# Performance work log

Measured on AMD Instinct MI355X. Metric: run time of the kernel, lower is better.

## Reference

```python
import jax, jax.numpy as jnp
import numpy as np

N = 8192          # num nodes
T = 8             # num node types (== num_bases, full basis)
H = 4             # attention heads
IN = 64           # in_feat
OUT = 64          # out_feat


def setup_inputs() -> dict:
    key = jax.random.key(0)
    ks = jax.random.split(key, 9)
    return {
        "agg_msg": jax.random.normal(ks[0], (N, H * IN), dtype=jnp.float32),
        "h": jax.random.normal(ks[1], (N, OUT), dtype=jnp.float32),
        "node_type": jax.random.randint(ks[2], (N,), 0, T),
        "W_att": jax.random.normal(ks[3], (T, H * IN, IN), dtype=jnp.float32) * 0.05,
        "b_att": jax.random.normal(ks[4], (T, OUT), dtype=jnp.float32) * 0.05,
        "W_in": jax.random.normal(ks[5], (T, IN, 3 * OUT), dtype=jnp.float32) * 0.05,
        "W_hid": jax.random.normal(ks[6], (T, OUT, 3 * OUT), dtype=jnp.float32) * 0.05,
        "b_in": jax.random.normal(ks[7], (T, 3 * OUT), dtype=jnp.float32) * 0.05,
        "b_hid": jax.random.normal(ks[8], (T, 3 * OUT), dtype=jnp.float32) * 0.05,
    }


def reference(agg_msg, h, node_type, W_att, b_att, W_in, W_hid, b_in, b_hid):
    # activation on aggregated message (F.relu)
    x = jax.nn.relu(agg_msg)                                 # [N, H*IN]
    # --- attention-head aggregation: per-node-type weight gather + bmm ---
    Wa = W_att[node_type]                                    # [N, H*IN, IN]  (irregular gather)
    x = jnp.einsum('nd,ndo->no', x, Wa) + b_att[node_type]   # [N, IN]
    x = jax.nn.relu(x)
    # --- GRU-style gated update with per-node-type weights ---
    gi = jnp.einsum('ni,nio->no', x, W_in[node_type]) + b_in[node_type]    # [N, 3*OUT]
    gh = jnp.einsum('nk,nko->no', h, W_hid[node_type]) + b_hid[node_type]  # [N, 3*OUT]
    i_r, i_z, i_n = jnp.split(gi, 3, axis=-1)
    h_r, h_z, h_n = jnp.split(gh, 3, axis=-1)
    r = jax.nn.sigmoid(i_r + h_r)
    z = jax.nn.sigmoid(i_z + h_z)
    n = jnp.tanh(i_n + r * h_n)
    h_new = (1.0 - z) * n + z * h                            # [N, OUT]
    return h_new
```

## Files before the change

### kernel.cpp

```cpp
#include <hip/hip_runtime.h>

#define N_NODES 8192
#define T_TYPES 8
#define HIN 256
#define OUTF 64
#define G3 192
#define BM 64
#define MAXBLK 135
#define SCAT_BLKS 32

typedef __attribute__((ext_vector_type(8))) __bf16 bf16x8;
typedef __attribute__((ext_vector_type(4))) float f32x4;

#define WS_CURS 0
#define WS_PERM 256
#define WS_WAT  (256 + 262144)
#define WS_WIT  (WS_WAT + 262144)
#define WS_WHT  (WS_WIT + 196608)
#define WS_CNT  (WS_WHT + 196608)

#define L_XS  0
#define L_WAS 32768
#define L_WIS 65536
#define L_WHS 90112
#define L_YS  114688
#define L_HS  122880
#define L_HF  131072
#define L_IDX 147456
#define L_TOT 147712

#define GLD_LDS16(g, l) __builtin_amdgcn_global_load_lds( \
    (const __attribute__((address_space(1))) void*)(g),   \
    (__attribute__((address_space(3))) void*)(l), 16, 0, 0)

__device__ __forceinline__ unsigned short f2bf(float f) {
    unsigned u = __float_as_uint(f);
    return (unsigned short)((u + 0x7FFFu + ((u >> 16) & 1u)) >> 16);
}
__device__ __forceinline__ int pack2bf(float a, float b) {
    return (int)f2bf(a) | ((int)f2bf(b) << 16);
}

__global__ __launch_bounds__(256) void prep_and_count(
    const float* __restrict__ W_att, const float* __restrict__ W_in,
    const float* __restrict__ W_hid, const int* __restrict__ nt,
    int* __restrict__ counts,
    unsigned short* __restrict__ waT, unsigned short* __restrict__ wiT,
    unsigned short* __restrict__ whT)
{
    __shared__ float Lf[64][68];
    __shared__ int hist[8];
    const int tid = threadIdx.x;
    const int b = blockIdx.x;

    if (b >= 80) {
        int j = b - 80;
        if (tid < 8) hist[tid] = 0;
        __syncthreads();
        atomicAdd(&hist[nt[j * 256 + tid]], 1);
        __syncthreads();
        if (tid < 8) counts[j * 8 + tid] = hist[tid];
        return;
    }

    const float* src;
    unsigned short* dstBase;
    int srcStride, rowBytes, colBase, rBase;

    if (b < 32) {
        int t = b >> 2, kt = b & 3;
        src = W_att + (((size_t)t * 256 + kt * 64) << 6);
        srcStride = 64;
        dstBase = waT + (size_t)t * 16384;
        rowBytes = 512; colBase = kt * 128; rBase = 0;
    } else {
        int j = b - 32;
        int isWh = (j >= 24); if (isWh) j -= 24;
        int t = j / 3, nt2 = j - t * 3;
        src = (isWh ? W_hid : W_in) + (size_t)t * 64 * 192 + nt2 * 64;
        srcStride = 192;
        dstBase = (isWh ? whT : wiT) + (size_t)t * 12288;
        rowBytes = 128; colBase = 0; rBase = nt2 * 64;
    }

    #pragma unroll
    for (int e = 0; e < 4; ++e) {
        int f = e * 256 + tid;
        int kk = f >> 4, c = (f & 15) << 2;
        float4 v = *(const float4*)(src + kk * srcStride + c);
        Lf[kk][c] = v.x; Lf[kk][c + 1] = v.y; Lf[kk][c + 2] = v.z; Lf[kk][c + 3] = v.w;
    }
    __syncthreads();

    #pragma unroll
    for (int e = 0; e < 2; ++e) {
        int q = e * 256 + tid;
        int ko8 = q >> 6, rl = q & 63;
        int r = rBase + rl;
        unsigned short tmp[8];
        #pragma unroll
        for (int j2 = 0; j2 < 8; ++j2)
            tmp[j2] = f2bf(Lf[ko8 * 8 + j2][rl]);
        int4 wv;
        wv.x = (int)tmp[0] | ((int)tmp[1] << 16);
        wv.y = (int)tmp[2] | ((int)tmp[3] << 16);
        wv.z = (int)tmp[4] | ((int)tmp[5] << 16);
        wv.w = (int)tmp[6] | ((int)tmp[7] << 16);
        int B = r * rowBytes + colBase + ((ko8 << 4) ^ ((r & 7) << 4));
        *(int4*)((char*)dstBase + B) = wv;
    }
}

__global__ __launch_bounds__(256) void scatter_pass(
    const int* __restrict__ nt, const int* __restrict__ counts,
    int* __restrict__ cursors, int* __restrict__ perm)
{
    __shared__ int tbl[SCAT_BLKS * 8];
    __shared__ int cur[8];
    const int tid = threadIdx.x;
    const int j = blockIdx.x;

    tbl[tid] = counts[tid];
    __syncthreads();
    if (tid < 8) {
        int base = 0, tot = 0;
        #pragma unroll
        for (int k = 0; k < SCAT_BLKS; ++k) {
            int c = tbl[k * 8 + tid];
            if (k < j) base += c;
            tot += c;
        }
        cur[tid] = base;
        if (j == 0) cursors[tid] = tot;
    }
    __syncthreads();
    int i = j * 256 + tid;
    int t = nt[i];
    int pos = atomicAdd(&cur[t], 1);
    perm[t * N_NODES + pos] = i;
}

__global__ __launch_bounds__(512, 1) void fused_rgnn(
    const float* __restrict__ agg, const float* __restrict__ h,
    const int* __restrict__ cursors, const int* __restrict__ perm,
    const unsigned short* __restrict__ waT, const unsigned short* __restrict__ wiT,
    const unsigned short* __restrict__ whT,
    const float* __restrict__ b_att, const float* __restrict__ b_in,
    const float* __restrict__ b_hid, float* __restrict__ out)
{
    __shared__ __align__(16) char sm_[L_TOT];
    char* sm = sm_;
    const int tid = threadIdx.x;
    const int b = blockIdx.x;

    const int4 c0 = *(const int4*)cursors;
    const int4 c1 = *(const int4*)(cursors + 4);
    const int cntArr[8] = {c0.x, c0.y, c0.z, c0.w, c1.x, c1.y, c1.z, c1.w};
    int t = -1, chunk = 0, tcnt = 0, acc = 0;
    #pragma unroll
    for (int tt = 0; tt < T_TYPES; ++tt) {
        int nc = (cntArr[tt] + BM - 1) >> 6;
        if (t < 0 && b < acc + nc) { t = tt; chunk = b - acc; tcnt = cntArr[tt]; }
        acc += nc;
    }
    if (t < 0) return;
    const int m0 = chunk * BM;
    const int mcnt = min(BM, tcnt - m0);

    const int lane = tid & 63;
    const int w = tid >> 6;
    const int wc = w & 3;
    const int wrh = w >> 2;
    const int lr = lane & 15;
    const int lk = lane >> 4;
    const int col = (wc << 4) + lr;
    const int swzA = (lr & 7) << 4;

    const float ba  = b_att[(t << 6) + col];
    const float bir = b_in [t * G3 + col];
    const float biz = b_in [t * G3 + 64 + col];
    const float bnn = b_in [t * G3 + 128 + col];
    const float bhr = b_hid[t * G3 + col];
    const float bhz = b_hid[t * G3 + 64 + col];
    const float bhn = b_hid[t * G3 + 128 + col];

    const int kx = (tid & 31) << 3;
    const int nbx = tid >> 5;
    int xg[4];
    #pragma unroll
    for (int s = 0; s < 4; ++s) {
        int node = nbx + (s << 4);
        xg[s] = (node < mcnt) ? perm[t * N_NODES + m0 + node] : -1;
    }
    const int nh = tid >> 3;
    const int kh = (tid & 7) << 3;
    int hg = (nh < mcnt) ? perm[t * N_NODES + m0 + nh] : -1;

    float4 xv[4][2];
    #pragma unroll
    for (int s = 0; s < 4; ++s) {
        if (xg[s] >= 0) {
            const float* p = agg + (size_t)xg[s] * HIN + kx;
            xv[s][0] = *(const float4*)p;
            xv[s][1] = *(const float4*)(p + 4);
        } else {
            xv[s][0] = make_float4(0.f, 0.f, 0.f, 0.f);
            xv[s][1] = make_float4(0.f, 0.f, 0.f, 0.f);
        }
    }
    float4 hv0, hv1;
    if (hg >= 0) {
        const float* p = h + (size_t)hg * OUTF + kh;
        hv0 = *(const float4*)p;
        hv1 = *(const float4*)(p + 4);
    } else {
        hv0 = make_float4(0.f, 0.f, 0.f, 0.f);
        hv1 = make_float4(0.f, 0.f, 0.f, 0.f);
    }

    {
        const char* was = (const char*)(waT + (size_t)t * 16384);
        const char* wis = (const char*)(wiT + (size_t)t * 12288);
        const char* whs = (const char*)(whT + (size_t)t * 12288);
        #pragma unroll
        for (int r = 0; r < 4; ++r) {
            int c = (r << 3) + w;
            GLD_LDS16(was + (c << 10) + (lane << 4), sm + L_WAS + (c << 10));
        }
        #pragma unroll
        for (int r = 0; r < 3; ++r) {
            int c = (r << 3) + w;
            GLD_LDS16(wis + (c << 10) + (lane << 4), sm + L_WIS + (c << 10));
            GLD_LDS16(whs + (c << 10) + (lane << 4), sm + L_WHS + (c << 10));
        }
    }

    #pragma unroll
    for (int s = 0; s < 4; ++s) {
        int node = nbx + (s << 4);
        float4 a = xv[s][0], bq = xv[s][1];
        int4 wv;
        wv.x = pack2bf(fmaxf(a.x, 0.f), fmaxf(a.y, 0.f));
        wv.y = pack2bf(fmaxf(a.z, 0.f), fmaxf(a.w, 0.f));
        wv.z = pack2bf(fmaxf(bq.x, 0.f), fmaxf(bq.y, 0.f));
        wv.w = pack2bf(fmaxf(bq.z, 0.f), fmaxf(bq.w, 0.f));
        *(int4*)(sm + L_XS + (node << 9) + ((kx << 1) ^ ((node & 7) << 4))) = wv;
    }
    {
        *(float4*)(sm + L_HF + (nh << 8) + (kh << 2)) = hv0;
        *(float4*)(sm + L_HF + (nh << 8) + (kh << 2) + 16) = hv1;
        int4 wv;
        wv.x = pack2bf(hv0.x, hv0.y);
        wv.y = pack2bf(hv0.z, hv0.w);
        wv.z = pack2bf(hv1.x, hv1.y);
        wv.w = pack2bf(hv1.z, hv1.w);
        *(int4*)(sm + L_HS + (nh << 7) + ((kh << 1) ^ ((nh & 7) << 4))) = wv;
        if ((tid & 7) == 0) ((int*)(sm + L_IDX))[nh] = hg;
    }
    __syncthreads();

    f32x4 yacc[2];
    #pragma unroll
    for (int m = 0; m < 2; ++m) yacc[m] = (f32x4){0.f, 0.f, 0.f, 0.f};
    #pragma unroll
    for (int ks = 0; ks < 8; ++ks) {
        int off = ((ks << 6) + (lk << 4)) ^ swzA;
        bf16x8 bb = *(const bf16x8*)(sm + L_WAS + (((wc << 4) + lr) << 9) + off);
        #pragma unroll
        for (int m = 0; m < 2; ++m) {
            int mt = (wrh << 1) + m;
            bf16x8 am = *(const bf16x8*)(sm + L_XS + (((mt << 4) + lr) << 9) + off);
            yacc[m] = __builtin_amdgcn_mfma_f32_16x16x32_bf16(am, bb, yacc[m], 0, 0, 0);
        }
    }
    #pragma unroll
    for (int m = 0; m < 2; ++m) {
        #pragma unroll
        for (int r = 0; r < 4; ++r) {
            int row = (((wrh << 1) + m) << 4) + (lk << 2) + r;
            float y = fmaxf(yacc[m][r] + ba, 0.f);
            *(unsigned short*)(sm + L_YS + (row << 7) +
                               ((col << 1) ^ ((row & 7) << 4))) = f2bf(y);
        }
    }
    __syncthreads();

    f32x4 gi[2][3], gh[2][3];
    #pragma unroll
    for (int m = 0; m < 2; ++m)
        #pragma unroll
        for (int g = 0; g < 3; ++g) {
            gi[m][g] = (f32x4){0.f, 0.f, 0.f, 0.f};
            gh[m][g] = (f32x4){0.f, 0.f, 0.f, 0.f};
        }
    #pragma unroll
    for (int ks = 0; ks < 2; ++ks) {
        int off = ((ks << 6) + (lk << 4)) ^ swzA;
        bf16x8 ay[2], ah[2];
        #pragma unroll
        for (int m = 0; m < 2; ++m) {
            int mt = (wrh << 1) + m;
            ay[m] = *(const bf16x8*)(sm + L_YS + (((mt << 4) + lr) << 7) + off);
            ah[m] = *(const bf16x8*)(sm + L_HS + (((mt << 4) + lr) << 7) + off);
        }
        #pragma unroll
        for (int g = 0; g < 3; ++g) {
            int brow = (g << 6) + col;
            bf16x8 bi = *(const bf16x8*)(sm + L_WIS + (brow << 7) + off);
            bf16x8 bh = *(const bf16x8*)(sm + L_WHS + (brow << 7) + off);
            #pragma unroll
            for (int m = 0; m < 2; ++m) {
                gi[m][g] = __builtin_amdgcn_mfma_f32_16x16x32_bf16(ay[m], bi, gi[m][g], 0, 0, 0);
                gh[m][g] = __builtin_amdgcn_mfma_f32_16x16x32_bf16(ah[m], bh, gh[m][g], 0, 0, 0);
            }
        }
    }

    const int* idxp = (const int*)(sm + L_IDX);
    #pragma unroll
    for (int m = 0; m < 2; ++m) {
        #pragma unroll
        for (int r = 0; r < 4; ++r) {
            int node = (((wrh << 1) + m) << 4) + (lk << 2) + r;
            if (node < mcnt) {
                int gidx = idxp[node];
                float rv = gi[m][0][r] + bir + gh[m][0][r] + bhr;
                float rg = 1.f / (1.f + __expf(-rv));
                float zv = gi[m][1][r] + biz + gh[m][1][r] + bhz;
                float zg = 1.f / (1.f + __expf(-zv));
                float ng = tanhf(gi[m][2][r] + bnn + rg * (gh[m][2][r] + bhn));
                float hold = *(const float*)(sm + L_HF + (node << 8) + (col << 2));
                out[(size_t)gidx * OUTF + col] = (1.f - zg) * ng + zg * hold;
            }
        }
    }
}

extern "C" void kernel_launch(void* const* d_in, const int* in_sizes, int n_in,
                              void* d_out, int out_size, void* d_ws, size_t ws_size,
                              hipStream_t stream) {
    const float* agg   = (const float*)d_in[0];
    const float* h     = (const float*)d_in[1];
    const int*   ntype = (const int*)d_in[2];
    const float* W_att = (const float*)d_in[3];
    const float* b_att = (const float*)d_in[4];
    const float* W_in  = (const float*)d_in[5];
    const float* W_hid = (const float*)d_in[6];
    const float* b_in  = (const float*)d_in[7];
    const float* b_hid = (const float*)d_in[8];
    float* out = (float*)d_out;

    char* ws = (char*)d_ws;
    int* cursors = (int*)(ws + WS_CURS);
    int* perm = (int*)(ws + WS_PERM);
    unsigned short* waT = (unsigned short*)(ws + WS_WAT);
    unsigned short* wiT = (unsigned short*)(ws + WS_WIT);
    unsigned short* whT = (unsigned short*)(ws + WS_WHT);
    int* counts = (int*)(ws + WS_CNT);

    prep_and_count<<<112, 256, 0, stream>>>(W_att, W_in, W_hid, ntype, counts, waT, wiT, whT);
    scatter_pass<<<SCAT_BLKS, 256, 0, stream>>>(ntype, counts, cursors, perm);
    fused_rgnn<<<MAXBLK, 512, 0, stream>>>(agg, h, cursors, perm,
        waT, wiT, whT, b_att, b_in, b_hid, out);
}
```

Measured before the change: 20.76 us.

## Fold scatter pass into fused kernel by building per-block index list in LDS

```diff
diff --git a/kernel.cpp b/kernel.cpp
--- a/kernel.cpp
+++ b/kernel.cpp
@@ -7,27 +7,28 @@
 #define G3 192
 #define BM 64
 #define MAXBLK 135
-#define SCAT_BLKS 32
 
 typedef __attribute__((ext_vector_type(8))) __bf16 bf16x8;
 typedef __attribute__((ext_vector_type(4))) float f32x4;
 
-#define WS_CURS 0
-#define WS_PERM 256
-#define WS_WAT  (256 + 262144)
+#define WS_CNT  0
+#define WS_WAT  1024
 #define WS_WIT  (WS_WAT + 262144)
 #define WS_WHT  (WS_WIT + 196608)
-#define WS_CNT  (WS_WHT + 196608)
-
-#define L_XS  0
-#define L_WAS 32768
-#define L_WIS 65536
-#define L_WHS 90112
-#define L_YS  114688
-#define L_HS  122880
-#define L_HF  131072
-#define L_IDX 147456
-#define L_TOT 147712
+
+#define L_XS   0
+#define L_WAS  32768
+#define L_WIS  65536
+#define L_WHS  90112
+#define L_YS   114688
+#define L_HS   122880
+#define L_HF   131072
+#define L_IDX  147456
+#define L_TBL  147712
+#define L_TOTS 148736
+#define L_SPRE 148768
+#define L_WCNT 148896
+#define L_TOT  148928
 
 #define GLD_LDS16(g, l) __builtin_amdgcn_global_load_lds( \
     (const __attribute__((address_space(1))) void*)(g),   \
@@ -111,38 +112,9 @@
     }
 }
 
-__global__ __launch_bounds__(256) void scatter_pass(
-    const int* __restrict__ nt, const int* __restrict__ counts,
-    int* __restrict__ cursors, int* __restrict__ perm)
-{
-    __shared__ int tbl[SCAT_BLKS * 8];
-    __shared__ int cur[8];
-    const int tid = threadIdx.x;
-    const int j = blockIdx.x;
-
-    tbl[tid] = counts[tid];
-    __syncthreads();
-    if (tid < 8) {
-        int base = 0, tot = 0;
-        #pragma unroll
-        for (int k = 0; k < SCAT_BLKS; ++k) {
-            int c = tbl[k * 8 + tid];
-            if (k < j) base += c;
-            tot += c;
-        }
-        cur[tid] = base;
-        if (j == 0) cursors[tid] = tot;
-    }
-    __syncthreads();
-    int i = j * 256 + tid;
-    int t = nt[i];
-    int pos = atomicAdd(&cur[t], 1);
-    perm[t * N_NODES + pos] = i;
-}
-
 __global__ __launch_bounds__(512, 1) void fused_rgnn(
     const float* __restrict__ agg, const float* __restrict__ h,
-    const int* __restrict__ cursors, const int* __restrict__ perm,
+    const int* __restrict__ nt, const int* __restrict__ counts,
     const unsigned short* __restrict__ waT, const unsigned short* __restrict__ wiT,
     const unsigned short* __restrict__ whT,
     const float* __restrict__ b_att, const float* __restrict__ b_in,
@@ -153,9 +125,22 @@
     const int tid = threadIdx.x;
     const int b = blockIdx.x;
 
-    const int4 c0 = *(const int4*)cursors;
-    const int4 c1 = *(const int4*)(cursors + 4);
-    const int cntArr[8] = {c0.x, c0.y, c0.z, c0.w, c1.x, c1.y, c1.z, c1.w};
+    int* tbl  = (int*)(sm + L_TBL);
+    int* tots = (int*)(sm + L_TOTS);
+    int* Spre = (int*)(sm + L_SPRE);
+    int* wcnt = (int*)(sm + L_WCNT);
+    if (tid < 256) tbl[tid] = counts[tid];
+    __syncthreads();
+    if (tid < 8) {
+        int s = 0;
+        #pragma unroll
+        for (int k = 0; k < 32; ++k) s += tbl[k * 8 + tid];
+        tots[tid] = s;
+    }
+    __syncthreads();
+    int cntArr[8];
+    #pragma unroll
+    for (int tt = 0; tt < 8; ++tt) cntArr[tt] = tots[tt];
     int t = -1, chunk = 0, tcnt = 0, acc = 0;
     #pragma unroll
     for (int tt = 0; tt < T_TYPES; ++tt) {
@@ -167,8 +152,36 @@
     const int m0 = chunk * BM;
     const int mcnt = min(BM, tcnt - m0);
 
+    if (tid < 32) {
+        int s = 0;
+        for (int k = 0; k < tid; ++k) s += tbl[k * 8 + t];
+        Spre[tid] = s;
+    }
+    __syncthreads();
+
+    int* idxLds = (int*)(sm + L_IDX);
     const int lane = tid & 63;
+    const unsigned long long below = (1ull << lane) - 1ull;
     const int w = tid >> 6;
+    for (int j = 0; j < 32; ++j) {
+        int Sj = Spre[j];
+        int cj = tbl[j * 8 + t];
+        if (Sj + cj <= m0 || Sj >= m0 + BM) continue;
+        bool ist = false;
+        if (tid < 256) ist = (nt[(j << 8) + tid] == t);
+        unsigned long long mask = __ballot(ist);
+        if (lane == 0 && w < 4) wcnt[w] = (int)__popcll(mask);
+        __syncthreads();
+        if (ist) {
+            int off = 0;
+            #pragma unroll
+            for (int k = 0; k < 4; ++k) if (k < w) off += wcnt[k];
+            int slot = Sj + off + (int)__popcll(mask & below) - m0;
+            if (slot >= 0 && slot < BM) idxLds[slot] = (j << 8) + tid;
+        }
+        __syncthreads();
+    }
+
     const int wc = w & 3;
     const int wrh = w >> 2;
     const int lr = lane & 15;
@@ -190,11 +203,11 @@
     #pragma unroll
     for (int s = 0; s < 4; ++s) {
         int node = nbx + (s << 4);
-        xg[s] = (node < mcnt) ? perm[t * N_NODES + m0 + node] : -1;
+        xg[s] = (node < mcnt) ? idxLds[node] : -1;
     }
     const int nh = tid >> 3;
     const int kh = (tid & 7) << 3;
-    int hg = (nh < mcnt) ? perm[t * N_NODES + m0 + nh] : -1;
+    int hg = (nh < mcnt) ? idxLds[nh] : -1;
 
     float4 xv[4][2];
     #pragma unroll
@@ -255,7 +268,6 @@
         wv.z = pack2bf(hv1.x, hv1.y);
         wv.w = pack2bf(hv1.z, hv1.w);
         *(int4*)(sm + L_HS + (nh << 7) + ((kh << 1) ^ ((nh & 7) << 4))) = wv;
-        if ((tid & 7) == 0) ((int*)(sm + L_IDX))[nh] = hg;
     }
     __syncthreads();
 
@@ -316,14 +328,13 @@
         }
     }
 
-    const int* idxp = (const int*)(sm + L_IDX);
     #pragma unroll
     for (int m = 0; m < 2; ++m) {
         #pragma unroll
         for (int r = 0; r < 4; ++r) {
             int node = (((wrh << 1) + m) << 4) + (lk << 2) + r;
             if (node < mcnt) {
-                int gidx = idxp[node];
+                int gidx = idxLds[node];
                 float rv = gi[m][0][r] + bir + gh[m][0][r] + bhr;
                 float rg = 1.f / (1.f + __expf(-rv));
                 float zv = gi[m][1][r] + biz + gh[m][1][r] + bhz;
@@ -351,15 +362,12 @@
     float* out = (float*)d_out;
 
     char* ws = (char*)d_ws;
-    int* cursors = (int*)(ws + WS_CURS);
-    int* perm = (int*)(ws + WS_PERM);
+    int* counts = (int*)(ws + WS_CNT);
     unsigned short* waT = (unsigned short*)(ws + WS_WAT);
     unsigned short* wiT = (unsigned short*)(ws + WS_WIT);
     unsigned short* whT = (unsigned short*)(ws + WS_WHT);
-    int* counts = (int*)(ws + WS_CNT);
 
     prep_and_count<<<112, 256, 0, stream>>>(W_att, W_in, W_hid, ntype, counts, waT, wiT, whT);
-    scatter_pass<<<SCAT_BLKS, 256, 0, stream>>>(ntype, counts, cursors, perm);
-    fused_rgnn<<<MAXBLK, 512, 0, stream>>>(agg, h, cursors, perm,
+    fused_rgnn<<<MAXBLK, 512, 0, stream>>>(agg, h, ntype, counts,
         waT, wiT, whT, b_att, b_in, b_hid, out);
 }
```

After: 22.21 us. +7.0%, slower.
